# Optimization experiments

Measured on AMD Instinct MI355X. Metric: run time of the kernel, lower is better.

Reference implementation:

```python
import jax, jax.numpy as jnp
import numpy as np


def _prelu(x, a):
    return jnp.where(x >= 0, x, a * x)


def setup_inputs() -> dict:
    key = jax.random.key(0)
    ks = jax.random.split(key, 10)
    B, N, h_dim, H_dim, g_dim, Kc, n = 64, 4096, 256, 1024, 512, 32, 2048
    hs = jax.random.normal(ks[0], (B, N, h_dim), dtype=jnp.float32)
    cs_o = jax.random.randint(ks[1], (B, N), 0, Kc, dtype=jnp.int32)

    def lin(k, fi, fo):
        return jax.random.normal(k, (fi, fo), dtype=jnp.float32) / np.sqrt(fi).astype(np.float32)

    a = jnp.full((1,), 0.25, dtype=jnp.float32)  # torch PReLU default
    return {
        "hs": hs,
        "W1": lin(ks[2], h_dim, H_dim), "b1": jnp.zeros((H_dim,), jnp.float32), "a1": a,
        "W2": lin(ks[3], H_dim, H_dim), "b2": jnp.zeros((H_dim,), jnp.float32), "a2": a,
        "W3": lin(ks[4], H_dim, H_dim), "b3": jnp.zeros((H_dim,), jnp.float32), "a3": a,
        "W4": lin(ks[5], H_dim, H_dim), "b4": jnp.zeros((H_dim,), jnp.float32), "a4": a,
        "W5": lin(ks[6], H_dim, H_dim), "b5": jnp.zeros((H_dim,), jnp.float32), "a5": a,
        "W6": lin(ks[7], H_dim, g_dim), "b6": jnp.zeros((g_dim,), jnp.float32),
        "cs_o": cs_o,
        "n": n,
    }


def reference(hs, W1, b1, a1, W2, b2, a2, W3, b3, a3, W4, b4, a4, W5, b5, a5, W6, b6, cs_o, n):
    B, N, h_dim = hs.shape
    cs = cs_o.at[:, n:].set(-1)                  # points >= n are unassigned
    K = int(jnp.max(cs)) + 1                      # static (concrete data)
    Ks = jnp.max(cs, axis=1)                      # [B] max cluster id per batch entry

    # per-cluster masked sums (vectorized segment-sum over all K at once)
    onehot = (cs[:, :, None] == jnp.arange(K)[None, None, :]).astype(hs.dtype)  # [B,N,K]
    Hk = jnp.einsum('bnk,bnh->bkh', onehot, hs)   # [B,K,h] sum of hs per cluster
    hn = hs[:, n, :]                              # [B,h] the point being assigned
    # H = [H_0..H_{K-1}, H_0+h_n..H_{K-1}+h_n, h_n]
    H = jnp.concatenate([Hk, Hk + hn[:, None, :], hn[:, None, :]], axis=1)  # [B,2K+1,h]

    mk = (jnp.sum(onehot, axis=1) > 0).astype(hs.dtype)  # [B,K] cluster non-empty
    gs_mask = jnp.concatenate([mk, mk, jnp.ones((B, 1), hs.dtype)], axis=1)[:, :, None]

    # 6-layer MLP g applied to all B*(2K+1) rows at once
    x = H.reshape(B * (2 * K + 1), h_dim)
    x = _prelu(x @ W1 + b1, a1)
    x = _prelu(x @ W2 + b2, a2)
    x = _prelu(x @ W3 + b3, a3)
    x = _prelu(x @ W4 + b4, a4)
    x = _prelu(x @ W5 + b5, a5)
    gs = (x @ W6 + b6).reshape(B, 2 * K + 1, -1) * gs_mask  # [B,2K+1,g]

    # G_k = sum_{j<K, j!=k} gs_j + gs_{k+K} ;  G_K = sum_{j<K} gs_j + gs_{2K}
    S = jnp.sum(gs[:, :K], axis=1)                                   # [B,g]
    G_head = (S[:, None, :] - gs[:, :K] + gs[:, K:2 * K]) * mk[:, :, None]
    G_last = S + gs[:, 2 * K]
    G = jnp.concatenate([G_head, G_last[:, None, :]], axis=1)        # [B,K+1,g]

    # per-batch correction: if Ks[b]==k (k<K-1), move G[b,-1] to slot k+1, zero last
    need = (Ks >= 0) & (Ks < K - 1)
    kidx = jnp.arange(K + 1)
    move = need[:, None] & (kidx[None, :] == (Ks + 1)[:, None])      # [B,K+1]
    G = jnp.where(move[:, :, None], G[:, K:K + 1, :], G)
    G = jnp.where((need[:, None] & (kidx[None, :] == K))[:, :, None], 0.0, G)
    G_mask = jnp.where(need[:, None] & (kidx[None, :] >= (Ks + 2)[:, None]),
                       0.0, jnp.ones((B, K + 1), hs.dtype))
    return (G, G_mask)
```

## Files before the change

kernel.cpp:

```cpp
#include <hip/hip_runtime.h>
#include <hip/hip_bf16.h>
#include <stdint.h>

using bf16x8 = __attribute__((ext_vector_type(8))) short;
using f32x4  = __attribute__((ext_vector_type(4))) float;

#define BATCH 64
#define NTOK  4096
#define HD    256
#define HDIM  1024
#define GD    512

__device__ __forceinline__ ushort f2bf(float f) {
  union { __hip_bfloat16 h; ushort u; } cv;
  cv.h = __float2bfloat16(f);
  return cv.u;
}

__device__ __forceinline__ void gload_lds16(const void* gsrc, void* ldst) {
  typedef const __attribute__((address_space(1))) uint32_t* gas_p;
  typedef __attribute__((address_space(3))) uint32_t* las_p;
  __builtin_amdgcn_global_load_lds((gas_p)(uintptr_t)gsrc, (las_p)(uintptr_t)ldst, 16, 0, 0);
}

struct WTArgs {
  const float* src[6];
  ushort* dst[6];
  int fi[6];
  int fo[6];
};

__global__ __launch_bounds__(256) void pre_kernel(WTArgs a,
                                                  const int* __restrict__ cs,
                                                  const int* __restrict__ nptr,
                                                  int* __restrict__ idx,
                                                  int* __restrict__ off,
                                                  int* __restrict__ cnt,
                                                  int* __restrict__ Ks,
                                                  int K) {
  __shared__ int csb[NTOK];
  __shared__ ushort hist[256 * 32];
  __shared__ int btot[32];
  __shared__ int bbase[32];
  __shared__ int red[4];
  __shared__ float tile[32][33];
  int t = threadIdx.x;
  if (blockIdx.x < BATCH) {
    int b = blockIdx.x;
    int n = *nptr;
    const int* csrow = cs + (size_t)b * NTOK;
    int mymax = -1;
    for (int i = t; i < n; i += 256) { int v = csrow[i]; csb[i] = v; mymax = max(mymax, v); }
#pragma unroll
    for (int k = 0; k < 32; ++k) hist[t * 32 + k] = 0;
    __syncthreads();
    int chunkN = (n + 255) >> 8;
    for (int c = 0; c < chunkN; ++c) {
      int i = c * 256 + t;
      if (i < n) hist[t * 32 + csb[i]]++;
    }
    __syncthreads();
    if (t < K) {
      int run = 0;
      for (int r = 0; r < 256; ++r) {
        int tmp = hist[r * 32 + t];
        hist[r * 32 + t] = (ushort)run;
        run += tmp;
      }
      btot[t] = run;
    }
    __syncthreads();
    if (t == 0) {
      int base = 0;
      for (int k = 0; k < K; ++k) { bbase[k] = base; base += btot[k]; }
    }
    __syncthreads();
    if (t < K) { off[b * K + t] = bbase[t]; cnt[b * K + t] = btot[t]; }
    int* idxb = idx + (size_t)b * NTOK;
    for (int c = 0; c < chunkN; ++c) {
      int i = c * 256 + t;
      if (i < n) {
        int k = csb[i];
        int s = bbase[k] + (int)(hist[t * 32 + k]++);
        idxb[s] = i;
      }
    }
    for (int o2 = 32; o2; o2 >>= 1) mymax = max(mymax, __shfl_down(mymax, o2));
    if ((t & 63) == 0) red[t >> 6] = mymax;
    __syncthreads();
    if (t == 0) {
      int r = red[0];
      for (int i = 1; i < 4; ++i) r = max(r, red[i]);
      Ks[b] = r;
    }
  } else {
    int f = blockIdx.x - BATCH;
    int z = 0;
    while (true) {
      int nb = (a.fo[z] >> 5) * (a.fi[z] >> 5);
      if (f < nb) break;
      f -= nb; ++z;
    }
    int ncx = a.fo[z] >> 5;
    int cx = f % ncx, cy = f / ncx;
    int c0 = cx * 32, r0 = cy * 32;
    int fo = a.fo[z], fi = a.fi[z];
    const float* W = a.src[z];
    ushort* Wt = a.dst[z];
    int tx = t & 31, ty = t >> 5;
#pragma unroll
    for (int j = 0; j < 4; ++j)
      tile[ty + j * 8][tx] = W[(size_t)(r0 + ty + j * 8) * fo + (c0 + tx)];
    __syncthreads();
#pragma unroll
    for (int j = 0; j < 4; ++j)
      Wt[(size_t)(c0 + ty + j * 8) * fi + (r0 + tx)] = f2bf(tile[tx][ty + j * 8]);
  }
}

__global__ __launch_bounds__(256) void aggregate2_kernel(const float* __restrict__ hs,
                                                         const int* __restrict__ idx,
                                                         const int* __restrict__ off,
                                                         const int* __restrict__ cnt,
                                                         const int* __restrict__ nptr,
                                                         ushort* __restrict__ X,
                                                         int K, int M, int Mpad) {
  int b = blockIdx.x / K, k = blockIdx.x % K;
  int t = threadIdx.x;
  int g = t >> 6, l = t & 63;
  int n = *nptr;
  int c = cnt[b * K + k];
  int o = off[b * K + k];
  const float* hsb = hs + (size_t)b * NTOK * HD;
  const int* ids = idx + (size_t)b * NTOK + o;
  __shared__ int sid[256];
  __shared__ float part[4][HD];
  float ax = 0.f, ay = 0.f, az = 0.f, aw = 0.f;
  float bx = 0.f, by = 0.f, bz = 0.f, bw = 0.f;
  for (int j0 = 0; j0 < c; j0 += 256) {
    __syncthreads();
    if (j0 + t < c) sid[t] = ids[j0 + t];
    __syncthreads();
    int lim = min(256, c - j0);
    int j = g;
    for (; j + 4 < lim; j += 8) {
      float4 v0 = ((const float4*)&hsb[(size_t)sid[j] * HD])[l];
      float4 v1 = ((const float4*)&hsb[(size_t)sid[j + 4] * HD])[l];
      ax += v0.x; ay += v0.y; az += v0.z; aw += v0.w;
      bx += v1.x; by += v1.y; bz += v1.z; bw += v1.w;
    }
    for (; j < lim; j += 4) {
      float4 v = ((const float4*)&hsb[(size_t)sid[j] * HD])[l];
      ax += v.x; ay += v.y; az += v.z; aw += v.w;
    }
  }
  part[g][l * 4 + 0] = ax + bx;
  part[g][l * 4 + 1] = ay + by;
  part[g][l * 4 + 2] = az + bz;
  part[g][l * 4 + 3] = aw + bw;
  __syncthreads();
  float sum = ((part[0][t] + part[1][t]) + (part[2][t] + part[3][t]));
  float hn = hsb[(size_t)n * HD + t];
  int R = 2 * K + 1;
  X[((size_t)b * R + k) * HD + t]     = f2bf(sum);
  X[((size_t)b * R + K + k) * HD + t] = f2bf(sum + hn);
  if (k == 0) {
    X[((size_t)b * R + 2 * K) * HD + t] = f2bf(hn);
    for (int r = M + b; r < Mpad; r += BATCH) X[(size_t)r * HD + t] = 0;
  }
}

template <bool LAST>
__global__ __launch_bounds__(256, 3) void gemm_kernel(const ushort* __restrict__ A,
                                                      const ushort* __restrict__ Bt,
                                                      const float* __restrict__ bias,
                                                      const float* __restrict__ aptr,
                                                      void* __restrict__ Cout,
                                                      int N, int Kd) {
  __shared__ ushort As[2][2][128 * 32];
  __shared__ ushort Bs[2][2][64 * 32];
  int tid = threadIdx.x;
  int lane = tid & 63, w = tid >> 6;
  int wr = w >> 1, wc = w & 1;
  int fr = lane & 15, fq = lane >> 4;

  int nwg = gridDim.x;
  int flat = blockIdx.x;
  int q8 = nwg >> 3, r8 = nwg & 7;
  int xcd = flat & 7, loc = flat >> 3;
  int swz = (xcd < r8 ? xcd * (q8 + 1) : r8 * (q8 + 1) + (xcd - r8) * q8) + loc;
  int NC = N >> 6;
  int brow = swz / NC, bcol = swz % NC;

  size_t row0 = (size_t)brow * 128;
  size_t col0 = (size_t)bcol * 64;

  const ushort* Abase = A + row0 * (size_t)Kd;
  const ushort* Bbase = Bt + col0 * (size_t)Kd;

  f32x4 acc[4][2] = {};

  int qA0 = w * 64 + lane;
  int qA1 = 256 + w * 64 + lane;
  int rA0 = qA0 >> 2, kA0 = (qA0 & 3) * 8;
  int rA1 = qA1 >> 2, kA1 = (qA1 & 3) * 8;
  int rB = qA0 >> 2, kB = (qA0 & 3) * 8;

  auto stage = [&](int buf, int k0) {
#pragma unroll
    for (int h = 0; h < 2; ++h) {
      int kh = k0 + h * 32;
      gload_lds16(Abase + (size_t)rA0 * Kd + kh + kA0, &As[buf][h][(w)     * 512]);
      gload_lds16(Abase + (size_t)rA1 * Kd + kh + kA1, &As[buf][h][(4 + w) * 512]);
      gload_lds16(Bbase + (size_t)rB  * Kd + kh + kB,  &Bs[buf][h][(w)     * 512]);
    }
  };

  int nt = Kd >> 6;
  int cur = 0;
  stage(0, 0);
  __syncthreads();
  for (int t = 0; t < nt; ++t) {
    if (t + 1 < nt) stage(cur ^ 1, (t + 1) * 64);
    bf16x8 af[2][4], bfv[2][2];
#pragma unroll
    for (int h = 0; h < 2; ++h) {
#pragma unroll
      for (int m = 0; m < 4; ++m)
        af[h][m] = *(const bf16x8*)&As[cur][h][(wr * 64 + m * 16 + fr) * 32 + fq * 8];
#pragma unroll
      for (int nn = 0; nn < 2; ++nn)
        bfv[h][nn] = *(const bf16x8*)&Bs[cur][h][(wc * 32 + nn * 16 + fr) * 32 + fq * 8];
    }
#pragma unroll
    for (int h = 0; h < 2; ++h)
#pragma unroll
      for (int m = 0; m < 4; ++m)
#pragma unroll
        for (int nn = 0; nn < 2; ++nn)
          acc[m][nn] = __builtin_amdgcn_mfma_f32_16x16x32_bf16(af[h][m], bfv[h][nn], acc[m][nn], 0, 0, 0);
    __syncthreads();
    cur ^= 1;
  }

  float alpha = 0.f;
  if (!LAST) alpha = aptr[0];
#pragma unroll
  for (int nn = 0; nn < 2; ++nn) {
    size_t col = col0 + wc * 32 + nn * 16 + fr;
    float bv = bias[col];
#pragma unroll
    for (int m = 0; m < 4; ++m) {
      size_t rbase = row0 + wr * 64 + m * 16 + fq * 4;
#pragma unroll
      for (int j = 0; j < 4; ++j) {
        float v = acc[m][nn][j] + bv;
        if (!LAST) {
          v = (v >= 0.f) ? v : alpha * v;
          ((ushort*)Cout)[(rbase + j) * N + col] = f2bf(v);
        } else {
          ((float*)Cout)[(rbase + j) * N + col] = v;
        }
      }
    }
  }
}

__global__ __launch_bounds__(256) void final_kernel(const float* __restrict__ gs,
                                                    const int* __restrict__ counts,
                                                    const int* __restrict__ Ks,
                                                    float* __restrict__ out,
                                                    int K) {
  int b = blockIdx.x, t = threadIdx.x;
  __shared__ float mk[64];
  __shared__ int sks;
  if (t < K) mk[t] = (counts[b * K + t] > 0) ? 1.f : 0.f;
  if (t == 0) sks = Ks[b];
  __syncthreads();
  int ks = sks;
  bool need = (ks >= 0) && (ks < K - 1);
  const float* g = gs + (size_t)b * (2 * K + 1) * GD;
  float S0 = 0.f, S1 = 0.f;
  for (int k = 0; k < K; ++k) {
    S0 += g[(size_t)k * GD + t] * mk[k];
    S1 += g[(size_t)k * GD + t + 256] * mk[k];
  }
  float gl0 = S0 + g[(size_t)(2 * K) * GD + t];
  float gl1 = S1 + g[(size_t)(2 * K) * GD + t + 256];
  float* G  = out + (size_t)b * (K + 1) * GD;
  float* Gm = out + (size_t)BATCH * (K + 1) * GD + (size_t)b * (K + 1);
  for (int kk = 0; kk <= K; ++kk) {
    float v0, v1;
    if (kk == K)                  { v0 = need ? 0.f : gl0; v1 = need ? 0.f : gl1; }
    else if (need && kk == ks + 1){ v0 = gl0;              v1 = gl1; }
    else {
      v0 = mk[kk] * (S0 - g[(size_t)kk * GD + t]       + g[(size_t)(K + kk) * GD + t]);
      v1 = mk[kk] * (S1 - g[(size_t)kk * GD + t + 256] + g[(size_t)(K + kk) * GD + t + 256]);
    }
    G[(size_t)kk * GD + t]       = v0;
    G[(size_t)kk * GD + t + 256] = v1;
  }
  if (t <= K) Gm[t] = (need && t >= ks + 2) ? 0.f : 1.f;
}

extern "C" void kernel_launch(void* const* d_in, const int* in_sizes, int n_in,
                              void* d_out, int out_size, void* d_ws, size_t ws_size,
                              hipStream_t stream) {
  const float* hs = (const float*)d_in[0];
  const float* W[6]  = {(const float*)d_in[1], (const float*)d_in[4], (const float*)d_in[7],
                        (const float*)d_in[10], (const float*)d_in[13], (const float*)d_in[16]};
  const float* bb[6] = {(const float*)d_in[2], (const float*)d_in[5], (const float*)d_in[8],
                        (const float*)d_in[11], (const float*)d_in[14], (const float*)d_in[17]};
  const float* aa[5] = {(const float*)d_in[3], (const float*)d_in[6], (const float*)d_in[9],
                        (const float*)d_in[12], (const float*)d_in[15]};
  const int* cs   = (const int*)d_in[18];
  const int* nptr = (const int*)d_in[19];
  float* out = (float*)d_out;

  int K = out_size / (BATCH * (GD + 1)) - 1;
  int M = BATCH * (2 * K + 1);
  int Mpad = (M + 127) / 128 * 128;

  char* base = (char*)d_ws;
  size_t off_b = 0;
  auto alloc = [&](size_t bytes) {
    char* p = base + off_b;
    off_b = (off_b + bytes + 255) & ~(size_t)255;
    return p;
  };
  ushort* W1t  = (ushort*)alloc((size_t)HDIM * HD * 2);
  ushort* W2t  = (ushort*)alloc((size_t)HDIM * HDIM * 2);
  ushort* W3t  = (ushort*)alloc((size_t)HDIM * HDIM * 2);
  ushort* W4t  = (ushort*)alloc((size_t)HDIM * HDIM * 2);
  ushort* W5bt = (ushort*)alloc((size_t)HDIM * HDIM * 2);
  ushort* W6t  = (ushort*)alloc((size_t)GD * HDIM * 2);
  int* idx     = (int*)alloc((size_t)BATCH * NTOK * 4);
  int* offb    = (int*)alloc((size_t)BATCH * K * 4);
  int* cntb    = (int*)alloc((size_t)BATCH * K * 4);
  int* Ksb     = (int*)alloc(BATCH * 4);
  ushort* X    = (ushort*)alloc((size_t)Mpad * HD * 2);
  ushort* Y0   = (ushort*)alloc((size_t)Mpad * HDIM * 2);
  ushort* Y1   = (ushort*)alloc((size_t)Mpad * HDIM * 2);
  float*  gsb  = (float*)alloc((size_t)Mpad * GD * 4);
  (void)ws_size; (void)n_in; (void)in_sizes;

  WTArgs wa;
  wa.src[0] = W[0]; wa.dst[0] = W1t;  wa.fi[0] = HD;   wa.fo[0] = HDIM;
  wa.src[1] = W[1]; wa.dst[1] = W2t;  wa.fi[1] = HDIM; wa.fo[1] = HDIM;
  wa.src[2] = W[2]; wa.dst[2] = W3t;  wa.fi[2] = HDIM; wa.fo[2] = HDIM;
  wa.src[3] = W[3]; wa.dst[3] = W4t;  wa.fi[3] = HDIM; wa.fo[3] = HDIM;
  wa.src[4] = W[4]; wa.dst[4] = W5bt; wa.fi[4] = HDIM; wa.fo[4] = HDIM;
  wa.src[5] = W[5]; wa.dst[5] = W6t;  wa.fi[5] = HDIM; wa.fo[5] = GD;
  int nbw = 0;
  for (int z = 0; z < 6; ++z) nbw += (wa.fo[z] / 32) * (wa.fi[z] / 32);
  hipLaunchKernelGGL(pre_kernel, dim3(BATCH + nbw), dim3(256), 0, stream,
                     wa, cs, nptr, idx, offb, cntb, Ksb, K);

  hipLaunchKernelGGL(aggregate2_kernel, dim3(BATCH * K), dim3(256), 0, stream,
                     hs, idx, offb, cntb, nptr, X, K, M, Mpad);

  dim3 blk(256);
  int NR = Mpad / 128;
  hipLaunchKernelGGL((gemm_kernel<false>), dim3(NR * (HDIM / 64)), blk, 0, stream, X,   W1t,  bb[0], aa[0], (void*)Y0, HDIM, HD);
  hipLaunchKernelGGL((gemm_kernel<false>), dim3(NR * (HDIM / 64)), blk, 0, stream, Y0,  W2t,  bb[1], aa[1], (void*)Y1, HDIM, HDIM);
  hipLaunchKernelGGL((gemm_kernel<false>), dim3(NR * (HDIM / 64)), blk, 0, stream, Y1,  W3t,  bb[2], aa[2], (void*)Y0, HDIM, HDIM);
  hipLaunchKernelGGL((gemm_kernel<false>), dim3(NR * (HDIM / 64)), blk, 0, stream, Y0,  W4t,  bb[3], aa[3], (void*)Y1, HDIM, HDIM);
  hipLaunchKernelGGL((gemm_kernel<false>), dim3(NR * (HDIM / 64)), blk, 0, stream, Y1,  W5bt, bb[4], aa[4], (void*)Y0, HDIM, HDIM);
  hipLaunchKernelGGL((gemm_kernel<true>),  dim3(NR * (GD / 64)),   blk, 0, stream, Y0,  W6t,  bb[5], nullptr, (void*)gsb, GD, HDIM);

  hipLaunchKernelGGL(final_kernel, dim3(BATCH), dim3(256), 0, stream, gsb, cntb, Ksb, out, K);
}
```

Measured before the change: 148.5 us.

## Retile GEMMs to 96-row tiles, parallelize histogram scan, widen aggregate and final kernels

```diff
diff --git a/kernel.cpp b/kernel.cpp
--- a/kernel.cpp
+++ b/kernel.cpp
@@ -40,6 +40,7 @@
                                                   int K) {
   __shared__ int csb[NTOK];
   __shared__ ushort hist[256 * 32];
+  __shared__ int segsum[8][32];
   __shared__ int btot[32];
   __shared__ int bbase[32];
   __shared__ int red[4];
@@ -60,16 +61,29 @@
       if (i < n) hist[t * 32 + csb[i]]++;
     }
     __syncthreads();
-    if (t < K) {
+    int kb = t & 31, sg = t >> 5;
+    {
       int run = 0;
-      for (int r = 0; r < 256; ++r) {
-        int tmp = hist[r * 32 + t];
-        hist[r * 32 + t] = (ushort)run;
+      int r0 = sg * 32;
+      for (int r = r0; r < r0 + 32; ++r) run += hist[r * 32 + kb];
+      segsum[sg][kb] = run;
+    }
+    __syncthreads();
+    if (t < 32) {
+      int acc0 = 0;
+      for (int s = 0; s < 8; ++s) { int v = segsum[s][t]; segsum[s][t] = acc0; acc0 += v; }
+      btot[t] = acc0;
+    }
+    __syncthreads();
+    {
+      int run = segsum[sg][kb];
+      int r0 = sg * 32;
+      for (int r = r0; r < r0 + 32; ++r) {
+        int tmp = hist[r * 32 + kb];
+        hist[r * 32 + kb] = (ushort)run;
         run += tmp;
       }
-      btot[t] = run;
-    }
-    __syncthreads();
+    }
     if (t == 0) {
       int base = 0;
       for (int k = 0; k < K; ++k) { bbase[k] = base; base += btot[k]; }
@@ -135,29 +149,35 @@
   const int* ids = idx + (size_t)b * NTOK + o;
   __shared__ int sid[256];
   __shared__ float part[4][HD];
-  float ax = 0.f, ay = 0.f, az = 0.f, aw = 0.f;
-  float bx = 0.f, by = 0.f, bz = 0.f, bw = 0.f;
+  float a0x = 0.f, a0y = 0.f, a0z = 0.f, a0w = 0.f;
+  float a1x = 0.f, a1y = 0.f, a1z = 0.f, a1w = 0.f;
+  float a2x = 0.f, a2y = 0.f, a2z = 0.f, a2w = 0.f;
+  float a3x = 0.f, a3y = 0.f, a3z = 0.f, a3w = 0.f;
   for (int j0 = 0; j0 < c; j0 += 256) {
     __syncthreads();
     if (j0 + t < c) sid[t] = ids[j0 + t];
     __syncthreads();
     int lim = min(256, c - j0);
     int j = g;
-    for (; j + 4 < lim; j += 8) {
+    for (; j + 12 < lim; j += 16) {
       float4 v0 = ((const float4*)&hsb[(size_t)sid[j] * HD])[l];
       float4 v1 = ((const float4*)&hsb[(size_t)sid[j + 4] * HD])[l];
-      ax += v0.x; ay += v0.y; az += v0.z; aw += v0.w;
-      bx += v1.x; by += v1.y; bz += v1.z; bw += v1.w;
+      float4 v2 = ((const float4*)&hsb[(size_t)sid[j + 8] * HD])[l];
+      float4 v3 = ((const float4*)&hsb[(size_t)sid[j + 12] * HD])[l];
+      a0x += v0.x; a0y += v0.y; a0z += v0.z; a0w += v0.w;
+      a1x += v1.x; a1y += v1.y; a1z += v1.z; a1w += v1.w;
+      a2x += v2.x; a2y += v2.y; a2z += v2.z; a2w += v2.w;
+      a3x += v3.x; a3y += v3.y; a3z += v3.z; a3w += v3.w;
     }
     for (; j < lim; j += 4) {
       float4 v = ((const float4*)&hsb[(size_t)sid[j] * HD])[l];
-      ax += v.x; ay += v.y; az += v.z; aw += v.w;
-    }
-  }
-  part[g][l * 4 + 0] = ax + bx;
-  part[g][l * 4 + 1] = ay + by;
-  part[g][l * 4 + 2] = az + bz;
-  part[g][l * 4 + 3] = aw + bw;
+      a0x += v.x; a0y += v.y; a0z += v.z; a0w += v.w;
+    }
+  }
+  part[g][l * 4 + 0] = (a0x + a1x) + (a2x + a3x);
+  part[g][l * 4 + 1] = (a0y + a1y) + (a2y + a3y);
+  part[g][l * 4 + 2] = (a0z + a1z) + (a2z + a3z);
+  part[g][l * 4 + 3] = (a0w + a1w) + (a2w + a3w);
   __syncthreads();
   float sum = ((part[0][t] + part[1][t]) + (part[2][t] + part[3][t]));
   float hn = hsb[(size_t)n * HD + t];
@@ -170,15 +190,15 @@
   }
 }
 
-template <bool LAST>
-__global__ __launch_bounds__(256, 3) void gemm_kernel(const ushort* __restrict__ A,
+template <int NN, bool LAST>
+__global__ __launch_bounds__(256, 4) void gemm_kernel(const ushort* __restrict__ A,
                                                       const ushort* __restrict__ Bt,
                                                       const float* __restrict__ bias,
                                                       const float* __restrict__ aptr,
                                                       void* __restrict__ Cout,
                                                       int N, int Kd) {
-  __shared__ ushort As[2][2][128 * 32];
-  __shared__ ushort Bs[2][2][64 * 32];
+  __shared__ ushort As[2][2][96 * 32];
+  __shared__ ushort Bs[2][2][NN * 32 * 32];
   int tid = threadIdx.x;
   int lane = tid & 63, w = tid >> 6;
   int wr = w >> 1, wc = w & 1;
@@ -189,16 +209,16 @@
   int q8 = nwg >> 3, r8 = nwg & 7;
   int xcd = flat & 7, loc = flat >> 3;
   int swz = (xcd < r8 ? xcd * (q8 + 1) : r8 * (q8 + 1) + (xcd - r8) * q8) + loc;
-  int NC = N >> 6;
+  int NC = N / (NN * 32);
   int brow = swz / NC, bcol = swz % NC;
 
-  size_t row0 = (size_t)brow * 128;
-  size_t col0 = (size_t)bcol * 64;
+  size_t row0 = (size_t)brow * 96;
+  size_t col0 = (size_t)bcol * (NN * 32);
 
   const ushort* Abase = A + row0 * (size_t)Kd;
   const ushort* Bbase = Bt + col0 * (size_t)Kd;
 
-  f32x4 acc[4][2] = {};
+  f32x4 acc[3][NN] = {};
 
   int qA0 = w * 64 + lane;
   int qA1 = 256 + w * 64 + lane;
@@ -210,9 +230,15 @@
 #pragma unroll
     for (int h = 0; h < 2; ++h) {
       int kh = k0 + h * 32;
-      gload_lds16(Abase + (size_t)rA0 * Kd + kh + kA0, &As[buf][h][(w)     * 512]);
-      gload_lds16(Abase + (size_t)rA1 * Kd + kh + kA1, &As[buf][h][(4 + w) * 512]);
-      gload_lds16(Bbase + (size_t)rB  * Kd + kh + kB,  &Bs[buf][h][(w)     * 512]);
+      gload_lds16(Abase + (size_t)rA0 * Kd + kh + kA0, &As[buf][h][(w * 64) * 8]);
+      if (w < 2)
+        gload_lds16(Abase + (size_t)rA1 * Kd + kh + kA1, &As[buf][h][(256 + w * 64) * 8]);
+      if (NN == 2) {
+        gload_lds16(Bbase + (size_t)rB * Kd + kh + kB, &Bs[buf][h][(w * 64) * 8]);
+      } else {
+        if (w < 2)
+          gload_lds16(Bbase + (size_t)rB * Kd + kh + kB, &Bs[buf][h][(w * 64) * 8]);
+      }
     }
   };
 
@@ -222,22 +248,22 @@
   __syncthreads();
   for (int t = 0; t < nt; ++t) {
     if (t + 1 < nt) stage(cur ^ 1, (t + 1) * 64);
-    bf16x8 af[2][4], bfv[2][2];
+    bf16x8 af[2][3], bfv[2][NN];
 #pragma unroll
     for (int h = 0; h < 2; ++h) {
 #pragma unroll
-      for (int m = 0; m < 4; ++m)
-        af[h][m] = *(const bf16x8*)&As[cur][h][(wr * 64 + m * 16 + fr) * 32 + fq * 8];
-#pragma unroll
-      for (int nn = 0; nn < 2; ++nn)
-        bfv[h][nn] = *(const bf16x8*)&Bs[cur][h][(wc * 32 + nn * 16 + fr) * 32 + fq * 8];
+      for (int m = 0; m < 3; ++m)
+        af[h][m] = *(const bf16x8*)&As[cur][h][(wr * 48 + m * 16 + fr) * 32 + fq * 8];
+#pragma unroll
+      for (int nn = 0; nn < NN; ++nn)
+        bfv[h][nn] = *(const bf16x8*)&Bs[cur][h][(wc * (NN * 16) + nn * 16 + fr) * 32 + fq * 8];
     }
 #pragma unroll
     for (int h = 0; h < 2; ++h)
 #pragma unroll
-      for (int m = 0; m < 4; ++m)
-#pragma unroll
-        for (int nn = 0; nn < 2; ++nn)
+      for (int m = 0; m < 3; ++m)
+#pragma unroll
+        for (int nn = 0; nn < NN; ++nn)
           acc[m][nn] = __builtin_amdgcn_mfma_f32_16x16x32_bf16(af[h][m], bfv[h][nn], acc[m][nn], 0, 0, 0);
     __syncthreads();
     cur ^= 1;
@@ -246,12 +272,12 @@
   float alpha = 0.f;
   if (!LAST) alpha = aptr[0];
 #pragma unroll
-  for (int nn = 0; nn < 2; ++nn) {
-    size_t col = col0 + wc * 32 + nn * 16 + fr;
+  for (int nn = 0; nn < NN; ++nn) {
+    size_t col = col0 + wc * (NN * 16) + nn * 16 + fr;
     float bv = bias[col];
 #pragma unroll
-    for (int m = 0; m < 4; ++m) {
-      size_t rbase = row0 + wr * 64 + m * 16 + fq * 4;
+    for (int m = 0; m < 3; ++m) {
+      size_t rbase = row0 + wr * 48 + m * 16 + fq * 4;
 #pragma unroll
       for (int j = 0; j < 4; ++j) {
         float v = acc[m][nn][j] + bv;
@@ -271,7 +297,9 @@
                                                     const int* __restrict__ Ks,
                                                     float* __restrict__ out,
                                                     int K) {
-  int b = blockIdx.x, t = threadIdx.x;
+  int b = blockIdx.x >> 1, half = blockIdx.x & 1;
+  int t = threadIdx.x;
+  int col = half * 256 + t;
   __shared__ float mk[64];
   __shared__ int sks;
   if (t < K) mk[t] = (counts[b * K + t] > 0) ? 1.f : 0.f;
@@ -280,27 +308,19 @@
   int ks = sks;
   bool need = (ks >= 0) && (ks < K - 1);
   const float* g = gs + (size_t)b * (2 * K + 1) * GD;
-  float S0 = 0.f, S1 = 0.f;
-  for (int k = 0; k < K; ++k) {
-    S0 += g[(size_t)k * GD + t] * mk[k];
-    S1 += g[(size_t)k * GD + t + 256] * mk[k];
-  }
-  float gl0 = S0 + g[(size_t)(2 * K) * GD + t];
-  float gl1 = S1 + g[(size_t)(2 * K) * GD + t + 256];
+  float S0 = 0.f;
+  for (int k = 0; k < K; ++k) S0 += g[(size_t)k * GD + col] * mk[k];
+  float gl0 = S0 + g[(size_t)(2 * K) * GD + col];
   float* G  = out + (size_t)b * (K + 1) * GD;
   float* Gm = out + (size_t)BATCH * (K + 1) * GD + (size_t)b * (K + 1);
   for (int kk = 0; kk <= K; ++kk) {
-    float v0, v1;
-    if (kk == K)                  { v0 = need ? 0.f : gl0; v1 = need ? 0.f : gl1; }
-    else if (need && kk == ks + 1){ v0 = gl0;              v1 = gl1; }
-    else {
-      v0 = mk[kk] * (S0 - g[(size_t)kk * GD + t]       + g[(size_t)(K + kk) * GD + t]);
-      v1 = mk[kk] * (S1 - g[(size_t)kk * GD + t + 256] + g[(size_t)(K + kk) * GD + t + 256]);
-    }
-    G[(size_t)kk * GD + t]       = v0;
-    G[(size_t)kk * GD + t + 256] = v1;
-  }
-  if (t <= K) Gm[t] = (need && t >= ks + 2) ? 0.f : 1.f;
+    float v0;
+    if (kk == K)                   v0 = need ? 0.f : gl0;
+    else if (need && kk == ks + 1) v0 = gl0;
+    else v0 = mk[kk] * (S0 - g[(size_t)kk * GD + col] + g[(size_t)(K + kk) * GD + col]);
+    G[(size_t)kk * GD + col] = v0;
+  }
+  if (half == 0 && t <= K) Gm[t] = (need && t >= ks + 2) ? 0.f : 1.f;
 }
 
 extern "C" void kernel_launch(void* const* d_in, const int* in_sizes, int n_in,
@@ -319,7 +339,7 @@
 
   int K = out_size / (BATCH * (GD + 1)) - 1;
   int M = BATCH * (2 * K + 1);
-  int Mpad = (M + 127) / 128 * 128;
+  int Mpad = (M + 95) / 96 * 96;
 
   char* base = (char*)d_ws;
   size_t off_b = 0;
@@ -360,13 +380,13 @@
                      hs, idx, offb, cntb, nptr, X, K, M, Mpad);
 
   dim3 blk(256);
-  int NR = Mpad / 128;
-  hipLaunchKernelGGL((gemm_kernel<false>), dim3(NR * (HDIM / 64)), blk, 0, stream, X,   W1t,  bb[0], aa[0], (void*)Y0, HDIM, HD);
-  hipLaunchKernelGGL((gemm_kernel<false>), dim3(NR * (HDIM / 64)), blk, 0, stream, Y0,  W2t,  bb[1], aa[1], (void*)Y1, HDIM, HDIM);
-  hipLaunchKernelGGL((gemm_kernel<false>), dim3(NR * (HDIM / 64)), blk, 0, stream, Y1,  W3t,  bb[2], aa[2], (void*)Y0, HDIM, HDIM);
-  hipLaunchKernelGGL((gemm_kernel<false>), dim3(NR * (HDIM / 64)), blk, 0, stream, Y0,  W4t,  bb[3], aa[3], (void*)Y1, HDIM, HDIM);
-  hipLaunchKernelGGL((gemm_kernel<false>), dim3(NR * (HDIM / 64)), blk, 0, stream, Y1,  W5bt, bb[4], aa[4], (void*)Y0, HDIM, HDIM);
-  hipLaunchKernelGGL((gemm_kernel<true>),  dim3(NR * (GD / 64)),   blk, 0, stream, Y0,  W6t,  bb[5], nullptr, (void*)gsb, GD, HDIM);
-
-  hipLaunchKernelGGL(final_kernel, dim3(BATCH), dim3(256), 0, stream, gsb, cntb, Ksb, out, K);
-}
+  int NR = Mpad / 96;
+  hipLaunchKernelGGL((gemm_kernel<2, false>), dim3(NR * (HDIM / 64)), blk, 0, stream, X,   W1t,  bb[0], aa[0], (void*)Y0, HDIM, HD);
+  hipLaunchKernelGGL((gemm_kernel<2, false>), dim3(NR * (HDIM / 64)), blk, 0, stream, Y0,  W2t,  bb[1], aa[1], (void*)Y1, HDIM, HDIM);
+  hipLaunchKernelGGL((gemm_kernel<2, false>), dim3(NR * (HDIM / 64)), blk, 0, stream, Y1,  W3t,  bb[2], aa[2], (void*)Y0, HDIM, HDIM);
+  hipLaunchKernelGGL((gemm_kernel<2, false>), dim3(NR * (HDIM / 64)), blk, 0, stream, Y0,  W4t,  bb[3], aa[3], (void*)Y1, HDIM, HDIM);
+  hipLaunchKernelGGL((gemm_kernel<2, false>), dim3(NR * (HDIM / 64)), blk, 0, stream, Y1,  W5bt, bb[4], aa[4], (void*)Y0, HDIM, HDIM);
+  hipLaunchKernelGGL((gemm_kernel<1, true>),  dim3(NR * (GD / 32)),   blk, 0, stream, Y0,  W6t,  bb[5], nullptr, (void*)gsb, GD, HDIM);
+
+  hipLaunchKernelGGL(final_kernel, dim3(BATCH * 2), dim3(256), 0, stream, gsb, cntb, Ksb, out, K);
+}
```

After: 135.8 us. -8.6%, faster.
